# Optimization experiments

Hardware: AMD Instinct MI355X
Metric: run time of the kernel (lower is better)

Reference implementation:

```python
import jax, jax.numpy as jnp
import numpy as np

DIM = 1024
H = 16
HD = DIM // H  # 64
EPS = 1e-6
B, N = 1, 2048


def setup_inputs() -> dict:
    key = jax.random.key(0)
    k1, k2, k3 = jax.random.split(key, 3)
    x = jax.random.normal(k1, (B, N, DIM), dtype=jnp.float32)
    qkv_w = jax.random.normal(k2, (3 * DIM, DIM), dtype=jnp.float32) * 0.02
    proj_w = jax.random.normal(k3, (DIM, DIM), dtype=jnp.float32) * 0.02
    alpha_log = jnp.zeros((H,), dtype=jnp.float32)  # torch init: zeros
    beta_log = jnp.zeros((H,), dtype=jnp.float32)
    return {"x": x, "qkv_w": qkv_w, "proj_w": proj_w,
            "alpha_log": alpha_log, "beta_log": beta_log}


def reference(x, qkv_w, proj_w, alpha_log, beta_log):
    b, n, c = x.shape
    # fused qkv projection (nn.Linear: y = x @ W.T), split into per-head q,k,v
    qkv = (x @ qkv_w.T).reshape(b, n, 3, H, HD).transpose(2, 0, 3, 1, 4)
    q, k, v = qkv[0], qkv[1], qkv[2]  # each [b,h,n,d]
    # positive ReLU feature map
    phi_q = jax.nn.relu(q) + EPS
    phi_k = jax.nn.relu(k) + EPS
    # causal prefix-sum of outer products phi_k v^T -> running state S_n
    kv = jnp.einsum('bhnd,bhne->bhnde', phi_k, v)   # [b,h,n,d,d]
    S = jnp.cumsum(kv, axis=2)                       # prefix sums over n
    out = jnp.einsum('bhnd,bhnde->bhne', phi_q, S)   # [b,h,n,d]
    # SteLLA normalization: per-head alpha'*beta'*sqrt(d) * prefix length
    alpha_p = jax.nn.softplus(alpha_log) + 1e-6
    beta_p = jax.nn.softplus(beta_log) + 1e-6
    scale = (alpha_p * beta_p * jnp.sqrt(jnp.float32(HD))).reshape(1, H, 1, 1)
    pos = jnp.arange(1, n + 1, dtype=x.dtype).reshape(1, 1, n, 1)
    denom = jnp.maximum(scale * pos, EPS)
    out = out / denom
    out = out.transpose(0, 2, 1, 3).reshape(b, n, c)
    return out @ proj_w.T  # output projection (dropout=0 -> identity)
```

## Files before the change

### kernel.cpp

```cpp
#include <hip/hip_runtime.h>
#include <math.h>

#define DIM 1024
#define NH 16
#define HD 64
#define SEQ 2048
#define CHUNK 128
#define NCHUNK (SEQ / CHUNK)
#define QKV_COLS (3 * DIM)

typedef __attribute__((ext_vector_type(8))) short bf16x8;
typedef __attribute__((ext_vector_type(4))) float f32x4;

__device__ __forceinline__ unsigned short f2bf(float f) {
  unsigned int u = __float_as_uint(f);
  u += 0x7FFF + ((u >> 16) & 1);
  return (unsigned short)(u >> 16);
}
__device__ __forceinline__ float bf2f(unsigned short s) {
  return __uint_as_float(((unsigned int)s) << 16);
}
__device__ __forceinline__ int swzb(int byte, int row) {
  return byte ^ ((row & 7) << 4);
}

__global__ __launch_bounds__(256) void convert_all(const float* __restrict__ x,
                                                   const float* __restrict__ qw,
                                                   const float* __restrict__ pw,
                                                   unsigned short* __restrict__ xb,
                                                   unsigned short* __restrict__ qwb,
                                                   unsigned short* __restrict__ pwb) {
  const int b = blockIdx.x;
  const float* in; unsigned short* out; int base;
  if (b < 512)       { in = x;  out = xb;  base = b * 1024; }
  else if (b < 1280) { in = qw; out = qwb; base = (b - 512) * 1024; }
  else               { in = pw; out = pwb; base = (b - 1280) * 1024; }
#pragma unroll
  for (int s = 0; s < 4; ++s) {
    const int i = base + s * 256 + threadIdx.x;
    float4 v = reinterpret_cast<const float4*>(in)[i];
    ushort4 o;
    o.x = f2bf(v.x); o.y = f2bf(v.y); o.z = f2bf(v.z); o.w = f2bf(v.w);
    reinterpret_cast<ushort4*>(out)[i] = o;
  }
}

template <int BM, int BN, int NBUF, bool PHI, typename OutT>
__global__ __launch_bounds__(256) void gemmN_bt(const unsigned short* __restrict__ A,
                                                const unsigned short* __restrict__ W,
                                                OutT* __restrict__ C,
                                                int M, int Nn, int K) {
  constexpr int BK = 32;
  constexpr int MFR = BM / 32;
  constexpr int NFR = BN / 32;
  constexpr int ACH = BM / 64;
  constexpr int BCH = BN / 64;
  constexpr int L = ACH + BCH;
  static_assert(L == 2 || L == 3, "vmcnt ladder assumes L in {2,3}");
  __shared__ unsigned short As[NBUF][BM * BK];
  __shared__ unsigned short Bs[NBUF][BN * BK];
  const int tid  = threadIdx.x;
  const int lane = tid & 63;
  const int wv   = tid >> 6;
  const int nwg  = gridDim.x * gridDim.y;
  int wgid = blockIdx.y * gridDim.x + blockIdx.x;
  wgid = (wgid & 7) * (nwg >> 3) + (wgid >> 3);
  const int row0 = (wgid / gridDim.x) * BM;
  const int col0 = (wgid % gridDim.x) * BN;
  const int ln15 = lane & 15;
  const int lhi  = lane >> 4;
  const int wr = (wv >> 1) * (BM / 2);
  const int wc = (wv & 1) * (BN / 2);

  f32x4 acc[MFR][NFR] = {};

  auto stage = [&](int buf, int t) {
    const int k0 = t * BK;
#pragma unroll
    for (int tt = 0; tt < ACH; ++tt) {
      const int chunk = wv * ACH + tt;
      const int lid = chunk * 64 + lane;
      const int r  = lid >> 2;
      const int ke = (lid & 3) << 3;
      __builtin_amdgcn_global_load_lds(
          (const __attribute__((address_space(1))) void*)&A[(size_t)(row0 + r) * K + k0 + ke],
          (__attribute__((address_space(3))) void*)&As[buf][chunk * 512], 16, 0, 0);
    }
#pragma unroll
    for (int tt = 0; tt < BCH; ++tt) {
      const int chunk = wv * BCH + tt;
      const int lid = chunk * 64 + lane;
      const int r  = lid >> 2;
      const int ke = (lid & 3) << 3;
      __builtin_amdgcn_global_load_lds(
          (const __attribute__((address_space(1))) void*)&W[(size_t)(col0 + r) * K + k0 + ke],
          (__attribute__((address_space(3))) void*)&Bs[buf][chunk * 512], 16, 0, 0);
    }
  };

  const int nt = K / BK;
#pragma unroll
  for (int i = 0; i < NBUF - 1; ++i) stage(i, i);
  for (int t = 0; t < nt; ++t) {
    const int k = (nt - 1 - t) < (NBUF - 2) ? (nt - 1 - t) : (NBUF - 2);
    if constexpr (L == 3) {
      switch (k) {
        case 4:  asm volatile("s_waitcnt vmcnt(12)" ::: "memory"); break;
        case 3:  asm volatile("s_waitcnt vmcnt(9)"  ::: "memory"); break;
        case 2:  asm volatile("s_waitcnt vmcnt(6)"  ::: "memory"); break;
        case 1:  asm volatile("s_waitcnt vmcnt(3)"  ::: "memory"); break;
        default: asm volatile("s_waitcnt vmcnt(0)"  ::: "memory"); break;
      }
    } else {
      switch (k) {
        case 4:  asm volatile("s_waitcnt vmcnt(8)"  ::: "memory"); break;
        case 3:  asm volatile("s_waitcnt vmcnt(6)"  ::: "memory"); break;
        case 2:  asm volatile("s_waitcnt vmcnt(4)"  ::: "memory"); break;
        case 1:  asm volatile("s_waitcnt vmcnt(2)"  ::: "memory"); break;
        default: asm volatile("s_waitcnt vmcnt(0)"  ::: "memory"); break;
      }
    }
    __builtin_amdgcn_s_barrier();
    if (t + NBUF - 1 < nt) stage((t + NBUF - 1) % NBUF, t + NBUF - 1);
    const int cur = t % NBUF;
    bf16x8 a[MFR], b[NFR];
#pragma unroll
    for (int m = 0; m < MFR; ++m)
      a[m] = *reinterpret_cast<const bf16x8*>(&As[cur][(wr + m * 16 + ln15) * BK + lhi * 8]);
#pragma unroll
    for (int n = 0; n < NFR; ++n)
      b[n] = *reinterpret_cast<const bf16x8*>(&Bs[cur][(wc + n * 16 + ln15) * BK + lhi * 8]);
#pragma unroll
    for (int m = 0; m < MFR; ++m)
#pragma unroll
      for (int n = 0; n < NFR; ++n)
        acc[m][n] = __builtin_amdgcn_mfma_f32_16x16x32_bf16(a[m], b[n], acc[m][n], 0, 0, 0);
  }

  const int crow = lhi * 4;
  const int ccol = ln15;
#pragma unroll
  for (int m = 0; m < MFR; ++m)
#pragma unroll
    for (int n = 0; n < NFR; ++n)
#pragma unroll
      for (int r = 0; r < 4; ++r) {
        const int gc = col0 + wc + n * 16 + ccol;
        float v = acc[m][n][r];
        if constexpr (PHI) {
          if (gc < 2 * DIM) v = fmaxf(v, 0.f) + 1e-6f;
        }
        const size_t idx = (size_t)(row0 + wr + m * 16 + crow + r) * Nn + gc;
        if constexpr (sizeof(OutT) == 2) C[idx] = (OutT)f2bf(v);
        else                             C[idx] = v;
      }
}

__global__ __launch_bounds__(256) void ckv_mfma_kernel(const unsigned short* __restrict__ qkv,
                                                       float* __restrict__ ckv) {
  const int h = blockIdx.x / NCHUNK;
  const int c = blockIdx.x % NCHUNK;
  const int tid  = threadIdx.x;
  const int lane = tid & 63;
  const int w    = tid >> 6;
  const int ln15 = lane & 15;
  const int lhi  = lane >> 4;

  __shared__ unsigned short kst[HD * CHUNK];
  __shared__ unsigned short vt[HD * CHUNK];

  for (int i = tid; i < CHUNK * HD / 4; i += 256) {
    const int r = i >> 4;
    const int d4 = (i & 15) << 2;
    const size_t base = (size_t)(c * CHUNK + r) * QKV_COLS + h * HD + d4;
    ushort4 k4 = *reinterpret_cast<const ushort4*>(&qkv[base + DIM]);
    ushort4 v4 = *reinterpret_cast<const ushort4*>(&qkv[base + 2 * DIM]);
#pragma unroll
    for (int j = 0; j < 4; ++j) {
      const int d = d4 + j;
      *reinterpret_cast<unsigned short*>((char*)kst + swzb(d * 256 + r * 2, d)) = (&k4.x)[j];
      *reinterpret_cast<unsigned short*>((char*)vt + swzb(d * 256 + r * 2, d)) = (&v4.x)[j];
    }
  }
  __syncthreads();

  f32x4 acc[4] = {};
#pragma unroll
  for (int ks = 0; ks < 4; ++ks) {
    const int dr = w * 16 + ln15;
    bf16x8 a = *reinterpret_cast<const bf16x8*>((char*)kst + swzb(dr * 256 + (ks * 32 + lhi * 8) * 2, dr));
#pragma unroll
    for (int et = 0; et < 4; ++et) {
      const int er = et * 16 + ln15;
      bf16x8 b = *reinterpret_cast<const bf16x8*>((char*)vt + swzb(er * 256 + (ks * 32 + lhi * 8) * 2, er));
      acc[et] = __builtin_amdgcn_mfma_f32_16x16x32_bf16(a, b, acc[et], 0, 0, 0);
    }
  }
  const size_t base = (size_t)(h * NCHUNK + c) * (HD * HD);
#pragma unroll
  for (int et = 0; et < 4; ++et)
#pragma unroll
    for (int r = 0; r < 4; ++r)
      ckv[base + (size_t)(w * 16 + lhi * 4 + r) * HD + et * 16 + ln15] = acc[et][r];
}

__global__ __launch_bounds__(256) void attn_mfma_kernel(const unsigned short* __restrict__ qkv,
                                                        const float* __restrict__ ckv,
                                                        const float* __restrict__ alpha_log,
                                                        const float* __restrict__ beta_log,
                                                        unsigned short* __restrict__ attn_out) {
  const int h = blockIdx.x / NCHUNK;
  const int c = blockIdx.x % NCHUNK;
  const int tid  = threadIdx.x;
  const int lane = tid & 63;
  const int w    = tid >> 6;
  const int ln15 = lane & 15;
  const int lhi  = lane >> 4;

  __shared__ unsigned short ks[CHUNK * HD];
  __shared__ unsigned short vst[HD * 256];
  __shared__ unsigned short ps[CHUNK * CHUNK];

  for (int i = tid; i < CHUNK * HD / 4; i += 256) {
    const int r = i >> 4;
    const int d4 = (i & 15) << 2;
    const size_t base = (size_t)(c * CHUNK + r) * QKV_COLS + h * HD + d4;
    ushort4 k4 = *reinterpret_cast<const ushort4*>(&qkv[base + DIM]);
    ushort4 v4 = *reinterpret_cast<const ushort4*>(&qkv[base + 2 * DIM]);
    *reinterpret_cast<ushort4*>((char*)ks + swzb(r * 128 + d4 * 2, r)) = k4;
#pragma unroll
    for (int j = 0; j < 4; ++j) {
      const int e = d4 + j;
      *reinterpret_cast<unsigned short*>((char*)vst + swzb(e * 512 + (128 + r) * 2, e)) = (&v4.x)[j];
    }
  }
  bf16x8 qf[2][2];
#pragma unroll
  for (int m = 0; m < 2; ++m)
#pragma unroll
    for (int kk = 0; kk < 2; ++kk) {
      const size_t gq = (size_t)(c * CHUNK + w * 32 + m * 16 + ln15) * QKV_COLS
                        + h * HD + kk * 32 + lhi * 8;
      qf[m][kk] = *reinterpret_cast<const bf16x8*>(&qkv[gq]);
    }

  {
    float sp[16];
#pragma unroll
    for (int p = 0; p < 16; ++p) sp[p] = 0.f;
    const float* cb = ckv + (size_t)h * NCHUNK * (HD * HD) + tid * 16;
    int cc = 0;
    for (; cc + 2 <= c; cc += 2) {
      const float4* pa = reinterpret_cast<const float4*>(cb + (size_t)cc * (HD * HD));
      const float4* pb = reinterpret_cast<const float4*>(cb + (size_t)(cc + 1) * (HD * HD));
#pragma unroll
      for (int q = 0; q < 4; ++q) {
        float4 t = pa[q];
        float4 u = pb[q];
        sp[q * 4 + 0] += t.x + u.x; sp[q * 4 + 1] += t.y + u.y;
        sp[q * 4 + 2] += t.z + u.z; sp[q * 4 + 3] += t.w + u.w;
      }
    }
    if (cc < c) {
      const float4* pa = reinterpret_cast<const float4*>(cb + (size_t)cc * (HD * HD));
#pragma unroll
      for (int q = 0; q < 4; ++q) {
        float4 t = pa[q];
        sp[q * 4 + 0] += t.x; sp[q * 4 + 1] += t.y;
        sp[q * 4 + 2] += t.z; sp[q * 4 + 3] += t.w;
      }
    }
    const int d = tid >> 2;
#pragma unroll
    for (int j = 0; j < 16; ++j) {
      const int e = (tid & 3) * 16 + j;
      const float sv = sp[j];
      const unsigned short hi = f2bf(sv);
      const unsigned short lo = f2bf(sv - bf2f(hi));
      *reinterpret_cast<unsigned short*>((char*)vst + swzb(e * 512 + d * 2, e)) = hi;
      *reinterpret_cast<unsigned short*>((char*)vst + swzb(e * 512 + (64 + d) * 2, e)) = lo;
    }
  }
  __syncthreads();

  f32x4 accs[2][8] = {};
#pragma unroll
  for (int j = 0; j < 8; ++j) {
    const int col = j * 16 + ln15;
    bf16x8 b0 = *reinterpret_cast<const bf16x8*>((char*)ks + swzb(col * 128 + lhi * 16, col));
    bf16x8 b1 = *reinterpret_cast<const bf16x8*>((char*)ks + swzb(col * 128 + 64 + lhi * 16, col));
#pragma unroll
    for (int m = 0; m < 2; ++m) {
      accs[m][j] = __builtin_amdgcn_mfma_f32_16x16x32_bf16(qf[m][0], b0, accs[m][j], 0, 0, 0);
      accs[m][j] = __builtin_amdgcn_mfma_f32_16x16x32_bf16(qf[m][1], b1, accs[m][j], 0, 0, 0);
    }
  }
#pragma unroll
  for (int m = 0; m < 2; ++m)
#pragma unroll
    for (int j = 0; j < 8; ++j)
#pragma unroll
      for (int r = 0; r < 4; ++r) {
        const int qrow = w * 32 + m * 16 + lhi * 4 + r;
        const int kcol = j * 16 + ln15;
        const float val = (qrow >= kcol) ? accs[m][j][r] : 0.f;
        *reinterpret_cast<unsigned short*>((char*)ps + swzb(qrow * 256 + kcol * 2, qrow)) = f2bf(val);
      }
  __syncthreads();

  f32x4 acco[2][4] = {};
#pragma unroll
  for (int kk = 0; kk < 8; ++kk) {
    bf16x8 a[2];
    if (kk < 4) {
#pragma unroll
      for (int m = 0; m < 2; ++m) a[m] = qf[m][kk & 1];
    } else {
#pragma unroll
      for (int m = 0; m < 2; ++m) {
        const int row = w * 32 + m * 16 + ln15;
        a[m] = *reinterpret_cast<const bf16x8*>((char*)ps + swzb(row * 256 + (kk - 4) * 64 + lhi * 16, row));
      }
    }
#pragma unroll
    for (int ct = 0; ct < 4; ++ct) {
      const int e = ct * 16 + ln15;
      bf16x8 b = *reinterpret_cast<const bf16x8*>((char*)vst + swzb(e * 512 + kk * 64 + lhi * 16, e));
#pragma unroll
      for (int m = 0; m < 2; ++m)
        acco[m][ct] = __builtin_amdgcn_mfma_f32_16x16x32_bf16(a[m], b, acco[m][ct], 0, 0, 0);
    }
  }

  const float ap = log1pf(expf(alpha_log[h])) + 1e-6f;
  const float bp = log1pf(expf(beta_log[h])) + 1e-6f;
  const float scale = ap * bp * 8.0f;
#pragma unroll
  for (int m = 0; m < 2; ++m)
#pragma unroll
    for (int ct = 0; ct < 4; ++ct)
#pragma unroll
      for (int r = 0; r < 4; ++r) {
        const int n = c * CHUNK + w * 32 + m * 16 + lhi * 4 + r;
        const float inv = 1.0f / fmaxf(scale * (float)(n + 1), 1e-6f);
        attn_out[(size_t)n * DIM + h * HD + ct * 16 + ln15] = f2bf(acco[m][ct][r] * inv);
      }
}

extern "C" void kernel_launch(void* const* d_in, const int* in_sizes, int n_in,
                              void* d_out, int out_size, void* d_ws, size_t ws_size,
                              hipStream_t stream) {
  const float* x        = (const float*)d_in[0];
  const float* qkv_w    = (const float*)d_in[1];
  const float* proj_w   = (const float*)d_in[2];
  const float* alpha_lg = (const float*)d_in[3];
  const float* beta_lg  = (const float*)d_in[4];
  float* out = (float*)d_out;

  char* ws = (char*)d_ws;
  size_t off = 0;
  unsigned short* qkvb = (unsigned short*)(ws + off); off += (size_t)SEQ * QKV_COLS * 2;
  float*          ckv  = (float*)         (ws + off); off += (size_t)NH * NCHUNK * HD * HD * 4;
  unsigned short* attn = (unsigned short*)(ws + off); off += (size_t)SEQ * DIM * 2;
  unsigned short* xb   = (unsigned short*)(ws + off); off += (size_t)SEQ * DIM * 2;
  unsigned short* qwb  = (unsigned short*)(ws + off); off += (size_t)QKV_COLS * DIM * 2;
  unsigned short* pwb  = (unsigned short*)(ws + off); off += (size_t)DIM * DIM * 2;

  convert_all<<<1536, 256, 0, stream>>>(x, qkv_w, proj_w, xb, qwb, pwb);
  gemmN_bt<64, 128, 4, true, unsigned short><<<dim3(QKV_COLS / 128, SEQ / 64), 256, 0, stream>>>(
      xb, qwb, qkvb, SEQ, QKV_COLS, DIM);
  ckv_mfma_kernel<<<NH * NCHUNK, 256, 0, stream>>>(qkvb, ckv);
  attn_mfma_kernel<<<NH * NCHUNK, 256, 0, stream>>>(qkvb, ckv, alpha_lg, beta_lg, attn);
  gemmN_bt<64, 64, 6, false, float><<<dim3(DIM / 64, SEQ / 64), 256, 0, stream>>>(
      attn, pwb, out, SEQ, DIM, DIM);
}
```

Baseline: 70.01 us.

## Split ckv and attention kernels into two blocks per chunk for more parallelism

Both chunk kernels now launch twice as many blocks: the ckv kernel splits the output columns of each chunk's K^T V product into two halves, and the attention kernel splits each 128-row chunk into two 64-row query halves. The aim is to raise occupancy across the GPU's CUs, since 256 blocks underfill the device. In exchange, each attention block still loads the full K/V chunk and re-sums the prefix state, so global traffic and redundant prefix-sum work double.

```diff
diff --git a/kernel.cpp b/kernel.cpp
--- a/kernel.cpp
+++ b/kernel.cpp
@@ -158,8 +158,10 @@
 
 __global__ __launch_bounds__(256) void ckv_mfma_kernel(const unsigned short* __restrict__ qkv,
                                                        float* __restrict__ ckv) {
-  const int h = blockIdx.x / NCHUNK;
-  const int c = blockIdx.x % NCHUNK;
+  const int b = blockIdx.x;
+  const int h  = b / (NCHUNK * 2);
+  const int c  = (b % (NCHUNK * 2)) >> 1;
+  const int eh = b & 1;
   const int tid  = threadIdx.x;
   const int lane = tid & 63;
   const int w    = tid >> 6;
@@ -167,41 +169,47 @@
   const int lhi  = lane >> 4;
 
   __shared__ unsigned short kst[HD * CHUNK];
-  __shared__ unsigned short vt[HD * CHUNK];
+  __shared__ unsigned short vt[(HD / 2) * CHUNK];
 
   for (int i = tid; i < CHUNK * HD / 4; i += 256) {
     const int r = i >> 4;
     const int d4 = (i & 15) << 2;
     const size_t base = (size_t)(c * CHUNK + r) * QKV_COLS + h * HD + d4;
     ushort4 k4 = *reinterpret_cast<const ushort4*>(&qkv[base + DIM]);
-    ushort4 v4 = *reinterpret_cast<const ushort4*>(&qkv[base + 2 * DIM]);
 #pragma unroll
     for (int j = 0; j < 4; ++j) {
       const int d = d4 + j;
       *reinterpret_cast<unsigned short*>((char*)kst + swzb(d * 256 + r * 2, d)) = (&k4.x)[j];
-      *reinterpret_cast<unsigned short*>((char*)vt + swzb(d * 256 + r * 2, d)) = (&v4.x)[j];
+    }
+    if ((d4 >> 5) == eh) {
+      ushort4 v4 = *reinterpret_cast<const ushort4*>(&qkv[base + 2 * DIM]);
+#pragma unroll
+      for (int j = 0; j < 4; ++j) {
+        const int el = (d4 & 31) + j;
+        *reinterpret_cast<unsigned short*>((char*)vt + swzb(el * 256 + r * 2, el)) = (&v4.x)[j];
+      }
     }
   }
   __syncthreads();
 
-  f32x4 acc[4] = {};
+  f32x4 acc[2] = {};
 #pragma unroll
   for (int ks = 0; ks < 4; ++ks) {
     const int dr = w * 16 + ln15;
     bf16x8 a = *reinterpret_cast<const bf16x8*>((char*)kst + swzb(dr * 256 + (ks * 32 + lhi * 8) * 2, dr));
 #pragma unroll
-    for (int et = 0; et < 4; ++et) {
+    for (int et = 0; et < 2; ++et) {
       const int er = et * 16 + ln15;
-      bf16x8 b = *reinterpret_cast<const bf16x8*>((char*)vt + swzb(er * 256 + (ks * 32 + lhi * 8) * 2, er));
-      acc[et] = __builtin_amdgcn_mfma_f32_16x16x32_bf16(a, b, acc[et], 0, 0, 0);
+      bf16x8 bb = *reinterpret_cast<const bf16x8*>((char*)vt + swzb(er * 256 + (ks * 32 + lhi * 8) * 2, er));
+      acc[et] = __builtin_amdgcn_mfma_f32_16x16x32_bf16(a, bb, acc[et], 0, 0, 0);
     }
   }
   const size_t base = (size_t)(h * NCHUNK + c) * (HD * HD);
 #pragma unroll
-  for (int et = 0; et < 4; ++et)
+  for (int et = 0; et < 2; ++et)
 #pragma unroll
     for (int r = 0; r < 4; ++r)
-      ckv[base + (size_t)(w * 16 + lhi * 4 + r) * HD + et * 16 + ln15] = acc[et][r];
+      ckv[base + (size_t)(w * 16 + lhi * 4 + r) * HD + eh * 32 + et * 16 + ln15] = acc[et][r];
 }
 
 __global__ __launch_bounds__(256) void attn_mfma_kernel(const unsigned short* __restrict__ qkv,
@@ -209,8 +217,10 @@
                                                         const float* __restrict__ alpha_log,
                                                         const float* __restrict__ beta_log,
                                                         unsigned short* __restrict__ attn_out) {
-  const int h = blockIdx.x / NCHUNK;
-  const int c = blockIdx.x % NCHUNK;
+  const int b = blockIdx.x;
+  const int h    = b / (NCHUNK * 2);
+  const int c    = (b % (NCHUNK * 2)) >> 1;
+  const int half = b & 1;
   const int tid  = threadIdx.x;
   const int lane = tid & 63;
   const int w    = tid >> 6;
@@ -219,7 +229,7 @@
 
   __shared__ unsigned short ks[CHUNK * HD];
   __shared__ unsigned short vst[HD * 256];
-  __shared__ unsigned short ps[CHUNK * CHUNK];
+  __shared__ unsigned short ps[64 * CHUNK];
 
   for (int i = tid; i < CHUNK * HD / 4; i += 256) {
     const int r = i >> 4;
@@ -234,15 +244,13 @@
       *reinterpret_cast<unsigned short*>((char*)vst + swzb(e * 512 + (128 + r) * 2, e)) = (&v4.x)[j];
     }
   }
-  bf16x8 qf[2][2];
-#pragma unroll
-  for (int m = 0; m < 2; ++m)
-#pragma unroll
-    for (int kk = 0; kk < 2; ++kk) {
-      const size_t gq = (size_t)(c * CHUNK + w * 32 + m * 16 + ln15) * QKV_COLS
-                        + h * HD + kk * 32 + lhi * 8;
-      qf[m][kk] = *reinterpret_cast<const bf16x8*>(&qkv[gq]);
-    }
+  bf16x8 qf[2];
+#pragma unroll
+  for (int kk = 0; kk < 2; ++kk) {
+    const size_t gq = (size_t)(c * CHUNK + half * 64 + w * 16 + ln15) * QKV_COLS
+                      + h * HD + kk * 32 + lhi * 8;
+    qf[kk] = *reinterpret_cast<const bf16x8*>(&qkv[gq]);
+  }
 
   {
     float sp[16];
@@ -283,52 +291,42 @@
   }
   __syncthreads();
 
-  f32x4 accs[2][8] = {};
+  f32x4 accs[8] = {};
 #pragma unroll
   for (int j = 0; j < 8; ++j) {
     const int col = j * 16 + ln15;
     bf16x8 b0 = *reinterpret_cast<const bf16x8*>((char*)ks + swzb(col * 128 + lhi * 16, col));
     bf16x8 b1 = *reinterpret_cast<const bf16x8*>((char*)ks + swzb(col * 128 + 64 + lhi * 16, col));
-#pragma unroll
-    for (int m = 0; m < 2; ++m) {
-      accs[m][j] = __builtin_amdgcn_mfma_f32_16x16x32_bf16(qf[m][0], b0, accs[m][j], 0, 0, 0);
-      accs[m][j] = __builtin_amdgcn_mfma_f32_16x16x32_bf16(qf[m][1], b1, accs[m][j], 0, 0, 0);
-    }
-  }
-#pragma unroll
-  for (int m = 0; m < 2; ++m)
-#pragma unroll
-    for (int j = 0; j < 8; ++j)
-#pragma unroll
-      for (int r = 0; r < 4; ++r) {
-        const int qrow = w * 32 + m * 16 + lhi * 4 + r;
-        const int kcol = j * 16 + ln15;
-        const float val = (qrow >= kcol) ? accs[m][j][r] : 0.f;
-        *reinterpret_cast<unsigned short*>((char*)ps + swzb(qrow * 256 + kcol * 2, qrow)) = f2bf(val);
-      }
+    accs[j] = __builtin_amdgcn_mfma_f32_16x16x32_bf16(qf[0], b0, accs[j], 0, 0, 0);
+    accs[j] = __builtin_amdgcn_mfma_f32_16x16x32_bf16(qf[1], b1, accs[j], 0, 0, 0);
+  }
+#pragma unroll
+  for (int j = 0; j < 8; ++j)
+#pragma unroll
+    for (int r = 0; r < 4; ++r) {
+      const int qrow_l = w * 16 + lhi * 4 + r;
+      const int qrow_g = half * 64 + qrow_l;
+      const int kcol = j * 16 + ln15;
+      const float val = (qrow_g >= kcol) ? accs[j][r] : 0.f;
+      *reinterpret_cast<unsigned short*>((char*)ps + swzb(qrow_l * 256 + kcol * 2, qrow_l)) = f2bf(val);
+    }
   __syncthreads();
 
-  f32x4 acco[2][4] = {};
+  f32x4 acco[4] = {};
 #pragma unroll
   for (int kk = 0; kk < 8; ++kk) {
-    bf16x8 a[2];
+    bf16x8 a;
     if (kk < 4) {
-#pragma unroll
-      for (int m = 0; m < 2; ++m) a[m] = qf[m][kk & 1];
+      a = qf[kk & 1];
     } else {
-#pragma unroll
-      for (int m = 0; m < 2; ++m) {
-        const int row = w * 32 + m * 16 + ln15;
-        a[m] = *reinterpret_cast<const bf16x8*>((char*)ps + swzb(row * 256 + (kk - 4) * 64 + lhi * 16, row));
-      }
+      const int row_l = w * 16 + ln15;
+      a = *reinterpret_cast<const bf16x8*>((char*)ps + swzb(row_l * 256 + (kk - 4) * 64 + lhi * 16, row_l));
     }
 #pragma unroll
     for (int ct = 0; ct < 4; ++ct) {
       const int e = ct * 16 + ln15;
-      bf16x8 b = *reinterpret_cast<const bf16x8*>((char*)vst + swzb(e * 512 + kk * 64 + lhi * 16, e));
-#pragma unroll
-      for (int m = 0; m < 2; ++m)
-        acco[m][ct] = __builtin_amdgcn_mfma_f32_16x16x32_bf16(a[m], b, acco[m][ct], 0, 0, 0);
+      bf16x8 bb = *reinterpret_cast<const bf16x8*>((char*)vst + swzb(e * 512 + kk * 64 + lhi * 16, e));
+      acco[ct] = __builtin_amdgcn_mfma_f32_16x16x32_bf16(a, bb, acco[ct], 0, 0, 0);
     }
   }
 
@@ -336,15 +334,13 @@
   const float bp = log1pf(expf(beta_log[h])) + 1e-6f;
   const float scale = ap * bp * 8.0f;
 #pragma unroll
-  for (int m = 0; m < 2; ++m)
-#pragma unroll
-    for (int ct = 0; ct < 4; ++ct)
-#pragma unroll
-      for (int r = 0; r < 4; ++r) {
-        const int n = c * CHUNK + w * 32 + m * 16 + lhi * 4 + r;
-        const float inv = 1.0f / fmaxf(scale * (float)(n + 1), 1e-6f);
-        attn_out[(size_t)n * DIM + h * HD + ct * 16 + ln15] = f2bf(acco[m][ct][r] * inv);
-      }
+  for (int ct = 0; ct < 4; ++ct)
+#pragma unroll
+    for (int r = 0; r < 4; ++r) {
+      const int n = c * CHUNK + half * 64 + w * 16 + lhi * 4 + r;
+      const float inv = 1.0f / fmaxf(scale * (float)(n + 1), 1e-6f);
+      attn_out[(size_t)n * DIM + h * HD + ct * 16 + ln15] = f2bf(acco[ct][r] * inv);
+    }
 }
 
 extern "C" void kernel_launch(void* const* d_in, const int* in_sizes, int n_in,
@@ -369,8 +365,8 @@
   convert_all<<<1536, 256, 0, stream>>>(x, qkv_w, proj_w, xb, qwb, pwb);
   gemmN_bt<64, 128, 4, true, unsigned short><<<dim3(QKV_COLS / 128, SEQ / 64), 256, 0, stream>>>(
       xb, qwb, qkvb, SEQ, QKV_COLS, DIM);
-  ckv_mfma_kernel<<<NH * NCHUNK, 256, 0, stream>>>(qkvb, ckv);
-  attn_mfma_kernel<<<NH * NCHUNK, 256, 0, stream>>>(qkvb, ckv, alpha_lg, beta_lg, attn);
+  ckv_mfma_kernel<<<NH * NCHUNK * 2, 256, 0, stream>>>(qkvb, ckv);
+  attn_mfma_kernel<<<NH * NCHUNK * 2, 256, 0, stream>>>(qkvb, ckv, alpha_lg, beta_lg, attn);
   gemmN_bt<64, 64, 6, false, float><<<dim3(DIM / 64, SEQ / 64), 256, 0, stream>>>(
       attn, pwb, out, SEQ, DIM, DIM);
 }
```

Measured after the change: 75.00 us. 7.1% more time.
